# Kernel tuning notes

Measured on AMD Instinct MI355X. Metric: run time of the kernel, lower is better.

## Reference

```python
import jax, jax.numpy as jnp
import numpy as np

C = 10  # cluster_num
EMB = 64

def setup_inputs() -> dict:
    key = jax.random.key(0)
    ks = jax.random.split(key, 12)
    B, N, D = 8, 4096, 1024
    n_classes = 1
    data = jax.random.normal(ks[0], (B, N, D), dtype=jnp.float32)
    labels = jax.random.randint(ks[1], (B, N), 0, C, dtype=jnp.int32)
    s = 0.02
    return {
        "data": data,
        "labels": labels,
        # embedding_net: Conv2d(1024,64,1) == linear on feature dim
        "W1": jax.random.normal(ks[2], (EMB, D), dtype=jnp.float32) * s,
        "b1": jnp.zeros((EMB,), dtype=jnp.float32),
        # attention MLP: Linear(64,32) -> tanh -> Linear(32,1)
        "Wa1": jax.random.normal(ks[3], (32, EMB), dtype=jnp.float32) * s,
        "ba1": jnp.zeros((32,), dtype=jnp.float32),
        "Wa2": jax.random.normal(ks[4], (1, 32), dtype=jnp.float32) * s,
        "ba2": jnp.zeros((1,), dtype=jnp.float32),
        # fc6: Linear(64,32) -> ReLU -> (Dropout eval=identity) -> Linear(32,n_classes)
        "Wf1": jax.random.normal(ks[5], (32, EMB), dtype=jnp.float32) * s,
        "bf1": jnp.zeros((32,), dtype=jnp.float32),
        "Wf2": jax.random.normal(ks[6], (n_classes, 32), dtype=jnp.float32) * s,
        "bf2": jnp.zeros((n_classes,), dtype=jnp.float32),
    }

def _masked_softmax(x, mask):
    # faithful to the module's numeric trick
    x_masked = x * mask + (1.0 - 1.0 / (mask + 1e-5))
    x_max = jnp.max(x_masked, axis=1, keepdims=True)
    x_exp = jnp.exp(x - x_max) * mask
    return x_exp / jnp.sum(x_exp, axis=1, keepdims=True)

def reference(data, labels, W1, b1, Wa1, ba1, Wa2, ba2, Wf1, bf1, Wf2, bf2):
    B, N, D = data.shape
    # per-patch 1x1-conv embed + ReLU: [B,N,64]
    e = jax.nn.relu(jnp.einsum('bnd,ed->bne', data, W1) + b1)
    # ragged per-cluster mean (AdaptiveAvgPool over each cluster's patches)
    seg = (labels.astype(jnp.int32) + jnp.arange(B, dtype=jnp.int32)[:, None] * C).reshape(-1)
    sums = jax.ops.segment_sum(e.reshape(B * N, EMB), seg, num_segments=B * C)
    counts = jax.ops.segment_sum(jnp.ones((B * N,), dtype=jnp.float32), seg, num_segments=B * C)
    sums = sums.reshape(B, C, EMB)
    counts = counts.reshape(B, C)
    mask = (counts > 0).astype(jnp.float32)
    h = sums / jnp.maximum(counts, 1.0)[..., None]  # [B,C,64]
    # attention scores over clusters
    a = jnp.einsum('bce,oe->bco', jnp.tanh(jnp.einsum('bce,he->bch', h, Wa1) + ba1), Wa2) + ba2
    A = _masked_softmax(a[..., 0], mask)  # [B,C]
    M = jnp.einsum('bc,bce->be', A, h)    # [B,64]
    # fc6 (dropout is identity at inference)
    logits = jax.nn.relu(M @ Wf1.T + bf1) @ Wf2.T + bf2
    return logits
```

## Files before the change

### kernel.cpp

```cpp
#include <hip/hip_runtime.h>

#define NC 10
#define EMB 64
#define DD 1024
#define NP 4096
#define NB 8

__global__ __launch_bounds__(512, 2) void embed_seg_kernel(
    const float* __restrict__ data, const int* __restrict__ labels,
    const float* __restrict__ W1, const float* __restrict__ b1,
    float* __restrict__ sums, float* __restrict__ counts)
{
    __shared__ float As[64][68];
    __shared__ float csum[NC][EMB];
    __shared__ float ccnt[NC];
    __shared__ int   labs[64];

    const int t    = threadIdx.x;
    const int lane = t & 63;
    const int w    = t >> 6;
    const int b    = blockIdx.x >> 6;
    const int p0   = (blockIdx.x & 63) << 6;

    for (int i = t; i < NC * EMB; i += 512) (&csum[0][0])[i] = 0.f;
    if (t < NC) ccnt[t] = 0.f;
    if (t < 64) labs[t] = labels[b * NP + p0 + t];

    const int we = __builtin_amdgcn_readfirstlane(w << 3);
    const float* __restrict__ Wb = W1 + (size_t)we * DD;

    const float* Ab = data + (size_t)(b * NP + p0) * DD;

    const int srow = t >> 3;
    const int scol = (t & 7) << 3;

    float acc[8] = {};

    for (int kk = 0; kk < DD; kk += 64) {
        __syncthreads();
        float4 v0 = *(const float4*)(Ab + (size_t)srow * DD + kk + scol);
        float4 v1 = *(const float4*)(Ab + (size_t)srow * DD + kk + scol + 4);
        *(float4*)&As[srow][scol]     = v0;
        *(float4*)&As[srow][scol + 4] = v1;
        __syncthreads();
#pragma unroll 2
        for (int kq = 0; kq < 16; ++kq) {
            const float4 av = *(const float4*)&As[lane][kq << 2];
#pragma unroll
            for (int e = 0; e < 8; ++e) {
                const float4 wv = *(const float4*)(Wb + (size_t)e * DD + kk + (kq << 2));
                acc[e] = fmaf(av.x, wv.x, acc[e]);
                acc[e] = fmaf(av.y, wv.y, acc[e]);
                acc[e] = fmaf(av.z, wv.z, acc[e]);
                acc[e] = fmaf(av.w, wv.w, acc[e]);
            }
        }
    }

    __syncthreads();
    const int lab = labs[lane];
#pragma unroll
    for (int e = 0; e < 8; ++e) {
        float vv = fmaxf(acc[e] + b1[we + e], 0.f);
        atomicAdd(&csum[lab][we + e], vv);
    }
    if (w == 0) atomicAdd(&ccnt[lab], 1.0f);
    __syncthreads();
    for (int i = t; i < NC * EMB; i += 512)
        atomicAdd(&sums[b * NC * EMB + i], (&csum[0][0])[i]);
    if (t < NC) atomicAdd(&counts[b * NC + t], ccnt[t]);
}

__global__ __launch_bounds__(128) void head_kernel(
    const float* __restrict__ sums, const float* __restrict__ counts,
    const float* __restrict__ Wa1, const float* __restrict__ ba1,
    const float* __restrict__ Wa2, const float* __restrict__ ba2,
    const float* __restrict__ Wf1, const float* __restrict__ bf1,
    const float* __restrict__ Wf2, const float* __restrict__ bf2,
    float* __restrict__ out)
{
    __shared__ float h[NC][EMB];
    __shared__ float mask[NC];
    __shared__ float att[NC][32];
    __shared__ float a_s[NC];
    __shared__ float A_s[NC];
    __shared__ float M_s[EMB];
    __shared__ float f_s[32];

    const int b = blockIdx.x;
    const int t = threadIdx.x;

    if (t < NC) {
        float cnt = counts[b * NC + t];
        mask[t] = cnt > 0.f ? 1.f : 0.f;
    }
    for (int i = t; i < NC * EMB; i += 128) {
        int c = i >> 6;
        float cnt = counts[b * NC + c];
        (&h[0][0])[i] = sums[b * NC * EMB + i] / fmaxf(cnt, 1.f);
    }
    __syncthreads();

    for (int task = t; task < NC * 32; task += 128) {
        int c = task >> 5, hh = task & 31;
        float s = ba1[hh];
        for (int e = 0; e < EMB; ++e) s = fmaf(Wa1[hh * EMB + e], h[c][e], s);
        att[c][hh] = tanhf(s);
    }
    __syncthreads();

    if (t < NC) {
        float s = ba2[0];
        for (int hh = 0; hh < 32; ++hh) s = fmaf(Wa2[hh], att[t][hh], s);
        a_s[t] = s;
    }
    __syncthreads();

    if (t == 0) {
        float xmax = -1e30f;
        for (int c = 0; c < NC; ++c) {
            float xm = a_s[c] * mask[c] + (1.0f - 1.0f / (mask[c] + 1e-5f));
            xmax = fmaxf(xmax, xm);
        }
        float ex[NC], ssum = 0.f;
        for (int c = 0; c < NC; ++c) {
            ex[c] = expf(a_s[c] - xmax) * mask[c];
            ssum += ex[c];
        }
        for (int c = 0; c < NC; ++c) A_s[c] = ex[c] / ssum;
    }
    __syncthreads();

    if (t < EMB) {
        float s = 0.f;
        for (int c = 0; c < NC; ++c) s = fmaf(A_s[c], h[c][t], s);
        M_s[t] = s;
    }
    __syncthreads();

    if (t < 32) {
        float s = bf1[t];
        for (int e = 0; e < EMB; ++e) s = fmaf(Wf1[t * EMB + e], M_s[e], s);
        f_s[t] = fmaxf(s, 0.f);
    }
    __syncthreads();

    if (t == 0) {
        float s = bf2[0];
        for (int hh = 0; hh < 32; ++hh) s = fmaf(Wf2[hh], f_s[hh], s);
        out[b] = s;
    }
}

extern "C" void kernel_launch(void* const* d_in, const int* in_sizes, int n_in,
                              void* d_out, int out_size, void* d_ws, size_t ws_size,
                              hipStream_t stream)
{
    const float* data   = (const float*)d_in[0];
    const int*   labels = (const int*)  d_in[1];
    const float* W1     = (const float*)d_in[2];
    const float* b1     = (const float*)d_in[3];
    const float* Wa1    = (const float*)d_in[4];
    const float* ba1    = (const float*)d_in[5];
    const float* Wa2    = (const float*)d_in[6];
    const float* ba2    = (const float*)d_in[7];
    const float* Wf1    = (const float*)d_in[8];
    const float* bf1    = (const float*)d_in[9];
    const float* Wf2    = (const float*)d_in[10];
    const float* bf2    = (const float*)d_in[11];

    float* sums   = (float*)d_ws;
    float* counts = sums + NB * NC * EMB;

    hipMemsetAsync(d_ws, 0, (size_t)(NB * NC * EMB + NB * NC) * sizeof(float), stream);

    embed_seg_kernel<<<NB * 64, 512, 0, stream>>>(data, labels, W1, b1, sums, counts);
    head_kernel<<<NB, 128, 0, stream>>>(sums, counts, Wa1, ba1, Wa2, ba2,
                                        Wf1, bf1, Wf2, bf2, (float*)d_out);
}
```

Before: 304.7 us.

## Double-buffer data tiles, prefetch W1 in registers, write per-block partials

Each block now covers 128 patches instead of 64, so every W1 register load is reused across two rows. The data tile is double-buffered in shared memory with a 32-wide K chunk, and W1 float4s are software-prefetched into registers one step ahead. The global atomics and the memset are replaced by per-block partial sums that the head kernel reduces, with the atomic path kept as a fallback when the workspace is too small. The aim is to hide global load latency and cut barrier and atomic overhead, at the cost of more registers under a higher occupancy target.

```diff
diff --git a/kernel.cpp b/kernel.cpp
--- a/kernel.cpp
+++ b/kernel.cpp
@@ -5,74 +5,118 @@
 #define DD 1024
 #define NP 4096
 #define NB 8
-
-__global__ __launch_bounds__(512, 2) void embed_seg_kernel(
+#define BP 128
+#define KC 32
+#define NCHUNK (DD / KC)
+#define SAS (KC + 4)
+#define NBLK (NB * NP / BP)
+#define PPB (NP / BP)
+
+__global__ __launch_bounds__(512, 4) void embed_seg_kernel(
     const float* __restrict__ data, const int* __restrict__ labels,
     const float* __restrict__ W1, const float* __restrict__ b1,
-    float* __restrict__ sums, float* __restrict__ counts)
+    float* __restrict__ psum, float* __restrict__ pcnt, int use_atomic)
 {
-    __shared__ float As[64][68];
+    __shared__ float As[2][BP][SAS];
     __shared__ float csum[NC][EMB];
     __shared__ float ccnt[NC];
-    __shared__ int   labs[64];
+    __shared__ int   labs[BP];
 
     const int t    = threadIdx.x;
     const int lane = t & 63;
     const int w    = t >> 6;
-    const int b    = blockIdx.x >> 6;
-    const int p0   = (blockIdx.x & 63) << 6;
+    const int bid  = blockIdx.x;
+    const int b    = bid >> 5;
+    const int p0   = (bid & 31) * BP;
 
     for (int i = t; i < NC * EMB; i += 512) (&csum[0][0])[i] = 0.f;
     if (t < NC) ccnt[t] = 0.f;
-    if (t < 64) labs[t] = labels[b * NP + p0 + t];
+    if (t < BP) labs[t] = labels[b * NP + p0 + t];
 
     const int we = __builtin_amdgcn_readfirstlane(w << 3);
-    const float* __restrict__ Wb = W1 + (size_t)we * DD;
-
-    const float* Ab = data + (size_t)(b * NP + p0) * DD;
-
-    const int srow = t >> 3;
-    const int scol = (t & 7) << 3;
-
-    float acc[8] = {};
-
-    for (int kk = 0; kk < DD; kk += 64) {
+    const float* __restrict__ Wbase = W1 + (size_t)we * DD;
+    const float* __restrict__ Ab    = data + (size_t)(b * NP + p0) * DD;
+
+    const int sp = t >> 3;
+    const int sk = (t & 7) << 2;
+
+    float4 sa0 = *(const float4*)(Ab + (size_t)sp * DD + sk);
+    float4 sa1 = *(const float4*)(Ab + (size_t)(sp + 64) * DD + sk);
+    *(float4*)&As[0][sp][sk]      = sa0;
+    *(float4*)&As[0][sp + 64][sk] = sa1;
+
+    float4 wreg[2][8];
+#pragma unroll
+    for (int e = 0; e < 8; ++e)
+        wreg[0][e] = *(const float4*)(Wbase + (size_t)e * DD);
+
+    float acc0[8] = {}, acc1[8] = {};
+    __syncthreads();
+
+    for (int c = 0; c < NCHUNK; ++c) {
+        const int buf = c & 1;
+        if (c + 1 < NCHUNK) {
+            sa0 = *(const float4*)(Ab + (size_t)sp * DD + (c + 1) * KC + sk);
+            sa1 = *(const float4*)(Ab + (size_t)(sp + 64) * DD + (c + 1) * KC + sk);
+        }
+#pragma unroll
+        for (int kq = 0; kq < 8; ++kq) {
+            const int cur = kq & 1, nxt = cur ^ 1;
+            const int gknext = c * KC + (kq + 1) * 4;
+            if (gknext < DD) {
+#pragma unroll
+                for (int e = 0; e < 8; ++e)
+                    wreg[nxt][e] = *(const float4*)(Wbase + (size_t)e * DD + gknext);
+            }
+            const float4 a0 = *(const float4*)&As[buf][lane][kq << 2];
+            const float4 a1 = *(const float4*)&As[buf][lane + 64][kq << 2];
+#pragma unroll
+            for (int e = 0; e < 8; ++e) {
+                const float4 wv = wreg[cur][e];
+                acc0[e] = fmaf(a0.x, wv.x, acc0[e]);
+                acc0[e] = fmaf(a0.y, wv.y, acc0[e]);
+                acc0[e] = fmaf(a0.z, wv.z, acc0[e]);
+                acc0[e] = fmaf(a0.w, wv.w, acc0[e]);
+                acc1[e] = fmaf(a1.x, wv.x, acc1[e]);
+                acc1[e] = fmaf(a1.y, wv.y, acc1[e]);
+                acc1[e] = fmaf(a1.z, wv.z, acc1[e]);
+                acc1[e] = fmaf(a1.w, wv.w, acc1[e]);
+            }
+        }
         __syncthreads();
-        float4 v0 = *(const float4*)(Ab + (size_t)srow * DD + kk + scol);
-        float4 v1 = *(const float4*)(Ab + (size_t)srow * DD + kk + scol + 4);
-        *(float4*)&As[srow][scol]     = v0;
-        *(float4*)&As[srow][scol + 4] = v1;
+        if (c + 1 < NCHUNK) {
+            *(float4*)&As[buf ^ 1][sp][sk]      = sa0;
+            *(float4*)&As[buf ^ 1][sp + 64][sk] = sa1;
+        }
         __syncthreads();
-#pragma unroll 2
-        for (int kq = 0; kq < 16; ++kq) {
-            const float4 av = *(const float4*)&As[lane][kq << 2];
-#pragma unroll
-            for (int e = 0; e < 8; ++e) {
-                const float4 wv = *(const float4*)(Wb + (size_t)e * DD + kk + (kq << 2));
-                acc[e] = fmaf(av.x, wv.x, acc[e]);
-                acc[e] = fmaf(av.y, wv.y, acc[e]);
-                acc[e] = fmaf(av.z, wv.z, acc[e]);
-                acc[e] = fmaf(av.w, wv.w, acc[e]);
-            }
-        }
-    }
-
-    __syncthreads();
-    const int lab = labs[lane];
+    }
+
+    const int lab0 = labs[lane], lab1 = labs[lane + 64];
 #pragma unroll
     for (int e = 0; e < 8; ++e) {
-        float vv = fmaxf(acc[e] + b1[we + e], 0.f);
-        atomicAdd(&csum[lab][we + e], vv);
-    }
-    if (w == 0) atomicAdd(&ccnt[lab], 1.0f);
-    __syncthreads();
-    for (int i = t; i < NC * EMB; i += 512)
-        atomicAdd(&sums[b * NC * EMB + i], (&csum[0][0])[i]);
-    if (t < NC) atomicAdd(&counts[b * NC + t], ccnt[t]);
+        const float bb = b1[we + e];
+        float v0 = fmaxf(acc0[e] + bb, 0.f);
+        float v1 = fmaxf(acc1[e] + bb, 0.f);
+        atomicAdd(&csum[lab0][we + e], v0);
+        atomicAdd(&csum[lab1][we + e], v1);
+    }
+    if (w == 0) atomicAdd(&ccnt[labs[lane]], 1.0f);
+    if (w == 1) atomicAdd(&ccnt[labs[lane + 64]], 1.0f);
+    __syncthreads();
+
+    if (use_atomic) {
+        for (int i = t; i < NC * EMB; i += 512)
+            atomicAdd(&psum[(size_t)b * NC * EMB + i], (&csum[0][0])[i]);
+        if (t < NC) atomicAdd(&pcnt[b * NC + t], ccnt[t]);
+    } else {
+        for (int i = t; i < NC * EMB; i += 512)
+            psum[(size_t)bid * NC * EMB + i] = (&csum[0][0])[i];
+        if (t < NC) pcnt[bid * NC + t] = ccnt[t];
+    }
 }
 
-__global__ __launch_bounds__(128) void head_kernel(
-    const float* __restrict__ sums, const float* __restrict__ counts,
+__global__ __launch_bounds__(256) void head_kernel(
+    const float* __restrict__ psum, const float* __restrict__ pcnt, int npb,
     const float* __restrict__ Wa1, const float* __restrict__ ba1,
     const float* __restrict__ Wa2, const float* __restrict__ ba2,
     const float* __restrict__ Wf1, const float* __restrict__ bf1,
@@ -80,6 +124,7 @@
     float* __restrict__ out)
 {
     __shared__ float h[NC][EMB];
+    __shared__ float cnt_s[NC];
     __shared__ float mask[NC];
     __shared__ float att[NC][32];
     __shared__ float a_s[NC];
@@ -91,17 +136,20 @@
     const int t = threadIdx.x;
 
     if (t < NC) {
-        float cnt = counts[b * NC + t];
-        mask[t] = cnt > 0.f ? 1.f : 0.f;
-    }
-    for (int i = t; i < NC * EMB; i += 128) {
-        int c = i >> 6;
-        float cnt = counts[b * NC + c];
-        (&h[0][0])[i] = sums[b * NC * EMB + i] / fmaxf(cnt, 1.f);
-    }
-    __syncthreads();
-
-    for (int task = t; task < NC * 32; task += 128) {
+        float s = 0.f;
+        for (int pb = 0; pb < npb; ++pb) s += pcnt[(size_t)(b * npb + pb) * NC + t];
+        cnt_s[t] = s;
+        mask[t]  = s > 0.f ? 1.f : 0.f;
+    }
+    __syncthreads();
+    for (int i = t; i < NC * EMB; i += 256) {
+        float s = 0.f;
+        for (int pb = 0; pb < npb; ++pb) s += psum[(size_t)(b * npb + pb) * NC * EMB + i];
+        (&h[0][0])[i] = s / fmaxf(cnt_s[i >> 6], 1.f);
+    }
+    __syncthreads();
+
+    for (int task = t; task < NC * 32; task += 256) {
         int c = task >> 5, hh = task & 31;
         float s = ba1[hh];
         for (int e = 0; e < EMB; ++e) s = fmaf(Wa1[hh * EMB + e], h[c][e], s);
@@ -169,12 +217,19 @@
     const float* Wf2    = (const float*)d_in[10];
     const float* bf2    = (const float*)d_in[11];
 
-    float* sums   = (float*)d_ws;
-    float* counts = sums + NB * NC * EMB;
-
-    hipMemsetAsync(d_ws, 0, (size_t)(NB * NC * EMB + NB * NC) * sizeof(float), stream);
-
-    embed_seg_kernel<<<NB * 64, 512, 0, stream>>>(data, labels, W1, b1, sums, counts);
-    head_kernel<<<NB, 128, 0, stream>>>(sums, counts, Wa1, ba1, Wa2, ba2,
-                                        Wf1, bf1, Wf2, bf2, (float*)d_out);
+    const size_t need = ((size_t)NBLK * NC * EMB + (size_t)NBLK * NC) * sizeof(float);
+    float* psum = (float*)d_ws;
+
+    if (ws_size >= need) {
+        float* pcnt = psum + (size_t)NBLK * NC * EMB;
+        embed_seg_kernel<<<NBLK, 512, 0, stream>>>(data, labels, W1, b1, psum, pcnt, 0);
+        head_kernel<<<NB, 256, 0, stream>>>(psum, pcnt, PPB, Wa1, ba1, Wa2, ba2,
+                                            Wf1, bf1, Wf2, bf2, (float*)d_out);
+    } else {
+        float* pcnt = psum + (size_t)NB * NC * EMB;
+        hipMemsetAsync(d_ws, 0, (size_t)(NB * NC * EMB + NB * NC) * sizeof(float), stream);
+        embed_seg_kernel<<<NBLK, 512, 0, stream>>>(data, labels, W1, b1, psum, pcnt, 1);
+        head_kernel<<<NB, 256, 0, stream>>>(psum, pcnt, 1, Wa1, ba1, Wa2, ba2,
+                                            Wf1, bf1, Wf2, bf2, (float*)d_out);
+    }
 }
```

Result: slower. 412.8 us (+35.5%).
